# Kernel tuning notes

Hardware: AMD Instinct MI355X
Metric: run time of the kernel (lower is better)

Reference implementation:

```python
import jax, jax.numpy as jnp
import numpy as np

TOP_K = 2


def setup_inputs() -> dict:
    key = jax.random.key(0)
    kx, kw = jax.random.split(key)
    B, S, D, E = 4, 4096, 2048, 64
    x = jax.random.normal(kx, (B, S, D), dtype=jnp.float32)
    W = jax.random.normal(kw, (E, D), dtype=jnp.float32) * 0.02  # router weight [E, D]
    return {"x": x, "W": W}


def reference(x, W):
    B, S, D = x.shape
    E = W.shape[0]
    x_flat = x.reshape(-1, D)                      # [T, D], T = B*S
    router_logits = jnp.einsum('td,ed->te', x_flat, W)  # [T, E]
    router_probs = jax.nn.softmax(router_logits, axis=-1)
    expert_weights, expert_indices = jax.lax.top_k(router_probs, TOP_K)  # [T, K]
    expert_weights = expert_weights / jnp.sum(expert_weights, axis=-1, keepdims=True)
    expert_indices = expert_indices.reshape(B, S, TOP_K)
    expert_weights = expert_weights.reshape(B, S, TOP_K)
    # aux load-balance loss: sum((mean usage - 1/E)^2)
    expert_usage = jnp.mean(router_probs, axis=0)  # [E]
    aux_loss = jnp.sum((expert_usage - 1.0 / E) ** 2)
    return expert_indices, expert_weights, aux_loss
```

## Files before the change

### kernel.cpp

```cpp
#include <hip/hip_runtime.h>
#include <math.h>

#define T_TOK 16384
#define DDIM  2048
#define NE    64
#define NPLANE (NE * DDIM)
#define NBLK  512

typedef __attribute__((ext_vector_type(8))) short short8;
typedef __attribute__((ext_vector_type(4))) float floatx4;

union Frag8 { unsigned short u[8]; short8 v; };

__device__ __forceinline__ unsigned int bf16_rne_bits(float x) {
    unsigned int u = __builtin_bit_cast(unsigned int, x);
    return (u + 0x7fffu + ((u >> 16) & 1u)) & 0xffff0000u;
}

__device__ __forceinline__ void dma16(const float* g, float* lds) {
    __builtin_amdgcn_global_load_lds(
        (const __attribute__((address_space(1))) unsigned int*)g,
        (__attribute__((address_space(3))) unsigned int*)lds, 16, 0, 0);
}

__global__ void wsplit_kernel(const float* __restrict__ W,
                              unsigned short* __restrict__ wh,
                              unsigned short* __restrict__ wm,
                              unsigned short* __restrict__ wl) {
    int i = blockIdx.x * 256 + threadIdx.x;
    float w = W[i];
    unsigned int hb = bf16_rne_bits(w);
    float r  = w - __builtin_bit_cast(float, hb);
    unsigned int mb = bf16_rne_bits(r);
    float r2 = r - __builtin_bit_cast(float, mb);
    unsigned int lb = bf16_rne_bits(r2);
    wh[i] = (unsigned short)(hb >> 16);
    wm[i] = (unsigned short)(mb >> 16);
    wl[i] = (unsigned short)(lb >> 16);
}

__global__ __launch_bounds__(512, 4)
void router_main(const float* __restrict__ x,
                 const unsigned short* __restrict__ wh,
                 const unsigned short* __restrict__ wm,
                 const unsigned short* __restrict__ wl,
                 float* __restrict__ out, float* __restrict__ usage_part) {
    __shared__ float As[2 * 8192];
    __shared__ float ured[8][NE];
    float* lg = As;

    const int tid  = threadIdx.x;
    const int lane = tid & 63;
    const int wv   = __builtin_amdgcn_readfirstlane(tid >> 6);
    const int nh   = wv & 1;
    const int kq   = wv >> 1;
    const int cl   = lane & 15;
    const int q    = lane >> 4;
    const int t0   = blockIdx.x * 32;

    const float* xdma = x + (size_t)(t0 + (lane & 31)) * DDIM + kq * 512 + (lane >> 5) * 4;

    floatx4 acc[2][2];
#pragma unroll
    for (int mt = 0; mt < 2; ++mt)
#pragma unroll
        for (int nt = 0; nt < 2; ++nt)
            acc[mt][nt] = (floatx4){0.f, 0.f, 0.f, 0.f};

    const size_t bbase = (size_t)(nh * 32 + cl) * DDIM + kq * 512 + q * 8;

#pragma unroll
    for (int j = 0; j < 4; ++j) {
        const int k8 = nh * 4 + j;
        dma16(xdma + k8 * 8, As + kq * 2048 + k8 * 256);
    }

#pragma unroll 1
    for (int c = 0; c < 8; ++c) {
        __syncthreads();

        if (c + 1 < 8) {
            float* nb = As + ((c + 1) & 1) * 8192 + kq * 2048;
#pragma unroll
            for (int j = 0; j < 4; ++j) {
                const int k8 = nh * 4 + j;
                dma16(xdma + (c + 1) * 64 + k8 * 8, nb + k8 * 256);
            }
        }

        const float* buf = As + (c & 1) * 8192 + kq * 2048;

#pragma unroll
        for (int t = 0; t < 2; ++t) {
            const size_t bo = bbase + c * 64 + t * 32;
            uint4 cb[2][3];
#pragma unroll
            for (int nt = 0; nt < 2; ++nt) {
                const size_t o = bo + (size_t)nt * 16 * DDIM;
                cb[nt][0] = *(const uint4*)(wh + o);
                cb[nt][1] = *(const uint4*)(wm + o);
                cb[nt][2] = *(const uint4*)(wl + o);
            }
            short8 Ah[2], Am[2], Al[2];
#pragma unroll
            for (int mt = 0; mt < 2; ++mt) {
                const float* ap = buf + (t * 4 + q) * 256 + (mt * 16 + cl) * 4;
                float4 a0 = *(const float4*)(ap);
                float4 a1 = *(const float4*)(ap + 128);
                float f[8] = {a0.x, a0.y, a0.z, a0.w, a1.x, a1.y, a1.z, a1.w};
                Frag8 fh, fm, fl;
#pragma unroll
                for (int j = 0; j < 8; ++j) {
                    unsigned int ub = __builtin_bit_cast(unsigned int, f[j]);
                    unsigned int hb = ub & 0xffff0000u;
                    float r = f[j] - __builtin_bit_cast(float, hb);
                    unsigned int rb = __builtin_bit_cast(unsigned int, r);
                    unsigned int mb = rb & 0xffff0000u;
                    float r2 = r - __builtin_bit_cast(float, mb);
                    unsigned int lb = __builtin_bit_cast(unsigned int, r2);
                    fh.u[j] = (unsigned short)(hb >> 16);
                    fm.u[j] = (unsigned short)(mb >> 16);
                    fl.u[j] = (unsigned short)(lb >> 16);
                }
                Ah[mt] = fh.v; Am[mt] = fm.v; Al[mt] = fl.v;
            }

#pragma unroll
            for (int mt = 0; mt < 2; ++mt)
#pragma unroll
                for (int nt = 0; nt < 2; ++nt) {
                    short8 Bh = __builtin_bit_cast(short8, cb[nt][0]);
                    short8 Bm = __builtin_bit_cast(short8, cb[nt][1]);
                    short8 Bl = __builtin_bit_cast(short8, cb[nt][2]);
                    floatx4 a = acc[mt][nt];
                    a = __builtin_amdgcn_mfma_f32_16x16x32_bf16(Ah[mt], Bh, a, 0, 0, 0);
                    a = __builtin_amdgcn_mfma_f32_16x16x32_bf16(Ah[mt], Bm, a, 0, 0, 0);
                    a = __builtin_amdgcn_mfma_f32_16x16x32_bf16(Am[mt], Bh, a, 0, 0, 0);
                    a = __builtin_amdgcn_mfma_f32_16x16x32_bf16(Am[mt], Bm, a, 0, 0, 0);
                    a = __builtin_amdgcn_mfma_f32_16x16x32_bf16(Ah[mt], Bl, a, 0, 0, 0);
                    a = __builtin_amdgcn_mfma_f32_16x16x32_bf16(Al[mt], Bh, a, 0, 0, 0);
                    acc[mt][nt] = a;
                }
        }
    }

#pragma unroll
    for (int mt = 0; mt < 2; ++mt)
#pragma unroll
        for (int nt = 0; nt < 2; ++nt)
#pragma unroll
            for (int r = 0; r < 4; ++r)
                lg[kq * 2048 + (mt * 16 + q * 4 + r) * 64 + nh * 32 + nt * 16 + cl]
                    = acc[mt][nt][r];
    __syncthreads();

    float usage_acc = 0.f;
#pragma unroll 1
    for (int j = 0; j < 4; ++j) {
        const int tl = wv * 4 + j;
        const int t  = t0 + tl;
        float l = (lg[0 * 2048 + tl * 64 + lane] + lg[1 * 2048 + tl * 64 + lane]) +
                  (lg[2 * 2048 + tl * 64 + lane] + lg[3 * 2048 + tl * 64 + lane]);

        float v1 = l; int i1 = lane;
#pragma unroll
        for (int off = 32; off >= 1; off >>= 1) {
            float ov = __shfl_xor(v1, off, 64);
            int   oi = __shfl_xor(i1, off, 64);
            if (ov > v1 || (ov == v1 && oi < i1)) { v1 = ov; i1 = oi; }
        }
        float lm = (lane == i1) ? -INFINITY : l;
        float v2 = lm; int i2 = lane;
#pragma unroll
        for (int off = 32; off >= 1; off >>= 1) {
            float ov = __shfl_xor(v2, off, 64);
            int   oi = __shfl_xor(i2, off, 64);
            if (ov > v2 || (ov == v2 && oi < i2)) { v2 = ov; i2 = oi; }
        }

        float p = expf(l - v1);
        float s = p;
#pragma unroll
        for (int off = 32; off >= 1; off >>= 1) s += __shfl_xor(s, off, 64);

        float e2  = expf(v2 - v1);
        float rcp = 1.0f / (1.0f + e2);
        usage_acc += p / s;

        if (lane == 0) {
            out[(size_t)t * 2 + 0]         = (float)i1;
            out[(size_t)t * 2 + 1]         = (float)i2;
            out[32768 + (size_t)t * 2 + 0] = rcp;
            out[32768 + (size_t)t * 2 + 1] = e2 * rcp;
        }
    }

    ured[wv][lane] = usage_acc;
    __syncthreads();
    if (wv == 0) {
        float s = ((ured[0][lane] + ured[1][lane]) + (ured[2][lane] + ured[3][lane])) +
                  ((ured[4][lane] + ured[5][lane]) + (ured[6][lane] + ured[7][lane]));
        usage_part[(size_t)blockIdx.x * 64 + lane] = s;
    }
}

__global__ __launch_bounds__(1024)
void router_aux(const float* __restrict__ usage_part, float* __restrict__ out) {
    __shared__ float red[16][NE];
    const int tid = threadIdx.x;
    const int e   = tid & 63;
    const int g   = tid >> 6;
    float s = 0.f;
#pragma unroll
    for (int i = 0; i < NBLK / 16; ++i)
        s += usage_part[(size_t)(g * (NBLK / 16) + i) * 64 + e];
    red[g][e] = s;
    __syncthreads();
    if (g == 0) {
        float tot = 0.f;
#pragma unroll
        for (int i = 0; i < 16; ++i) tot += red[i][e];
        float u = tot * (1.0f / 16384.0f) - (1.0f / 64.0f);
        float sq = u * u;
#pragma unroll
        for (int off = 32; off >= 1; off >>= 1) sq += __shfl_xor(sq, off, 64);
        if (e == 0) out[65536] = sq;
    }
}

extern "C" void kernel_launch(void* const* d_in, const int* in_sizes, int n_in,
                              void* d_out, int out_size, void* d_ws, size_t ws_size,
                              hipStream_t stream) {
    const float* x = (const float*)d_in[0];
    const float* W = (const float*)d_in[1];
    float* out     = (float*)d_out;

    unsigned short* ws_h = (unsigned short*)d_ws;
    unsigned short* ws_m = ws_h + NPLANE;
    unsigned short* ws_l = ws_m + NPLANE;
    float* upart         = (float*)(ws_l + NPLANE);

    wsplit_kernel<<<dim3(NPLANE / 256), dim3(256), 0, stream>>>(W, ws_h, ws_m, ws_l);
    router_main<<<dim3(NBLK), dim3(512), 0, stream>>>(x, ws_h, ws_m, ws_l, out, upart);
    router_aux<<<dim3(1), dim3(1024), 0, stream>>>(upart, out);
}
```

Baseline: 234.8 us.

## Load x directly from global into registers with 8-way K split per wave

Removes the LDS double-buffered global_load_lds staging of x and the per-chunk block barriers. Each of the 8 waves now owns a 256-wide K slice, reads its A fragments straight from global memory, and covers all 64 experts with a 2x4 accumulator tile. The 8 per-wave partial logits are then summed through LDS. This trades barrier and LDS traffic for uncoalesced 32-byte-per-lane global reads of x with no software prefetch, more accumulator registers, and a fully unrolled loop.

Result: slower. 243.8 us (+3.8%).

```diff
diff --git a/kernel.cpp b/kernel.cpp
--- a/kernel.cpp
+++ b/kernel.cpp
@@ -15,12 +15,6 @@
 __device__ __forceinline__ unsigned int bf16_rne_bits(float x) {
     unsigned int u = __builtin_bit_cast(unsigned int, x);
     return (u + 0x7fffu + ((u >> 16) & 1u)) & 0xffff0000u;
-}
-
-__device__ __forceinline__ void dma16(const float* g, float* lds) {
-    __builtin_amdgcn_global_load_lds(
-        (const __attribute__((address_space(1))) unsigned int*)g,
-        (__attribute__((address_space(3))) unsigned int*)lds, 16, 0, 0);
 }
 
 __global__ void wsplit_kernel(const float* __restrict__ W,
@@ -45,112 +39,88 @@
                  const unsigned short* __restrict__ wm,
                  const unsigned short* __restrict__ wl,
                  float* __restrict__ out, float* __restrict__ usage_part) {
-    __shared__ float As[2 * 8192];
+    __shared__ float lg[8 * 2048];
     __shared__ float ured[8][NE];
-    float* lg = As;
 
     const int tid  = threadIdx.x;
     const int lane = tid & 63;
     const int wv   = __builtin_amdgcn_readfirstlane(tid >> 6);
-    const int nh   = wv & 1;
-    const int kq   = wv >> 1;
     const int cl   = lane & 15;
     const int q    = lane >> 4;
     const int t0   = blockIdx.x * 32;
 
-    const float* xdma = x + (size_t)(t0 + (lane & 31)) * DDIM + kq * 512 + (lane >> 5) * 4;
-
-    floatx4 acc[2][2];
+    const float* xa = x + (size_t)(t0 + cl) * DDIM + wv * 256 + q * 8;
+    const size_t bb = (size_t)cl * DDIM + wv * 256 + q * 8;
+
+    floatx4 acc[2][4];
 #pragma unroll
     for (int mt = 0; mt < 2; ++mt)
 #pragma unroll
-        for (int nt = 0; nt < 2; ++nt)
+        for (int nt = 0; nt < 4; ++nt)
             acc[mt][nt] = (floatx4){0.f, 0.f, 0.f, 0.f};
 
-    const size_t bbase = (size_t)(nh * 32 + cl) * DDIM + kq * 512 + q * 8;
-
-#pragma unroll
-    for (int j = 0; j < 4; ++j) {
-        const int k8 = nh * 4 + j;
-        dma16(xdma + k8 * 8, As + kq * 2048 + k8 * 256);
-    }
-
-#pragma unroll 1
+#pragma unroll
     for (int c = 0; c < 8; ++c) {
-        __syncthreads();
-
-        if (c + 1 < 8) {
-            float* nb = As + ((c + 1) & 1) * 8192 + kq * 2048;
-#pragma unroll
-            for (int j = 0; j < 4; ++j) {
-                const int k8 = nh * 4 + j;
-                dma16(xdma + (c + 1) * 64 + k8 * 8, nb + k8 * 256);
+        const int ko = c * 32;
+
+        uint4 cb[4][3];
+#pragma unroll
+        for (int nt = 0; nt < 4; ++nt) {
+            const size_t o = bb + (size_t)nt * 16 * DDIM + ko;
+            cb[nt][0] = *(const uint4*)(wh + o);
+            cb[nt][1] = *(const uint4*)(wm + o);
+            cb[nt][2] = *(const uint4*)(wl + o);
+        }
+
+        short8 Ah[2], Am[2], Al[2];
+#pragma unroll
+        for (int mt = 0; mt < 2; ++mt) {
+            const float* ap = xa + (size_t)mt * 16 * DDIM + ko;
+            float4 a0 = *(const float4*)(ap);
+            float4 a1 = *(const float4*)(ap + 4);
+            float f[8] = {a0.x, a0.y, a0.z, a0.w, a1.x, a1.y, a1.z, a1.w};
+            Frag8 fh, fm, fl;
+#pragma unroll
+            for (int j = 0; j < 8; ++j) {
+                unsigned int ub = __builtin_bit_cast(unsigned int, f[j]);
+                unsigned int hb = ub & 0xffff0000u;
+                float r = f[j] - __builtin_bit_cast(float, hb);
+                unsigned int rb = __builtin_bit_cast(unsigned int, r);
+                unsigned int mb = rb & 0xffff0000u;
+                float r2 = r - __builtin_bit_cast(float, mb);
+                unsigned int lb = __builtin_bit_cast(unsigned int, r2);
+                fh.u[j] = (unsigned short)(hb >> 16);
+                fm.u[j] = (unsigned short)(mb >> 16);
+                fl.u[j] = (unsigned short)(lb >> 16);
             }
-        }
-
-        const float* buf = As + (c & 1) * 8192 + kq * 2048;
-
-#pragma unroll
-        for (int t = 0; t < 2; ++t) {
-            const size_t bo = bbase + c * 64 + t * 32;
-            uint4 cb[2][3];
-#pragma unroll
-            for (int nt = 0; nt < 2; ++nt) {
-                const size_t o = bo + (size_t)nt * 16 * DDIM;
-                cb[nt][0] = *(const uint4*)(wh + o);
-                cb[nt][1] = *(const uint4*)(wm + o);
-                cb[nt][2] = *(const uint4*)(wl + o);
+            Ah[mt] = fh.v; Am[mt] = fm.v; Al[mt] = fl.v;
+        }
+
+#pragma unroll
+        for (int mt = 0; mt < 2; ++mt)
+#pragma unroll
+            for (int nt = 0; nt < 4; ++nt) {
+                short8 Bh = __builtin_bit_cast(short8, cb[nt][0]);
+                short8 Bm = __builtin_bit_cast(short8, cb[nt][1]);
+                short8 Bl = __builtin_bit_cast(short8, cb[nt][2]);
+                floatx4 a = acc[mt][nt];
+                a = __builtin_amdgcn_mfma_f32_16x16x32_bf16(Ah[mt], Bh, a, 0, 0, 0);
+                a = __builtin_amdgcn_mfma_f32_16x16x32_bf16(Ah[mt], Bm, a, 0, 0, 0);
+                a = __builtin_amdgcn_mfma_f32_16x16x32_bf16(Am[mt], Bh, a, 0, 0, 0);
+                a = __builtin_amdgcn_mfma_f32_16x16x32_bf16(Am[mt], Bm, a, 0, 0, 0);
+                a = __builtin_amdgcn_mfma_f32_16x16x32_bf16(Ah[mt], Bl, a, 0, 0, 0);
+                a = __builtin_amdgcn_mfma_f32_16x16x32_bf16(Al[mt], Bh, a, 0, 0, 0);
+                acc[mt][nt] = a;
             }
-            short8 Ah[2], Am[2], Al[2];
-#pragma unroll
-            for (int mt = 0; mt < 2; ++mt) {
-                const float* ap = buf + (t * 4 + q) * 256 + (mt * 16 + cl) * 4;
-                float4 a0 = *(const float4*)(ap);
-                float4 a1 = *(const float4*)(ap + 128);
-                float f[8] = {a0.x, a0.y, a0.z, a0.w, a1.x, a1.y, a1.z, a1.w};
-                Frag8 fh, fm, fl;
-#pragma unroll
-                for (int j = 0; j < 8; ++j) {
-                    unsigned int ub = __builtin_bit_cast(unsigned int, f[j]);
-                    unsigned int hb = ub & 0xffff0000u;
-                    float r = f[j] - __builtin_bit_cast(float, hb);
-                    unsigned int rb = __builtin_bit_cast(unsigned int, r);
-                    unsigned int mb = rb & 0xffff0000u;
-                    float r2 = r - __builtin_bit_cast(float, mb);
-                    unsigned int lb = __builtin_bit_cast(unsigned int, r2);
-                    fh.u[j] = (unsigned short)(hb >> 16);
-                    fm.u[j] = (unsigned short)(mb >> 16);
-                    fl.u[j] = (unsigned short)(lb >> 16);
-                }
-                Ah[mt] = fh.v; Am[mt] = fm.v; Al[mt] = fl.v;
-            }
-
-#pragma unroll
-            for (int mt = 0; mt < 2; ++mt)
-#pragma unroll
-                for (int nt = 0; nt < 2; ++nt) {
-                    short8 Bh = __builtin_bit_cast(short8, cb[nt][0]);
-                    short8 Bm = __builtin_bit_cast(short8, cb[nt][1]);
-                    short8 Bl = __builtin_bit_cast(short8, cb[nt][2]);
-                    floatx4 a = acc[mt][nt];
-                    a = __builtin_amdgcn_mfma_f32_16x16x32_bf16(Ah[mt], Bh, a, 0, 0, 0);
-                    a = __builtin_amdgcn_mfma_f32_16x16x32_bf16(Ah[mt], Bm, a, 0, 0, 0);
-                    a = __builtin_amdgcn_mfma_f32_16x16x32_bf16(Am[mt], Bh, a, 0, 0, 0);
-                    a = __builtin_amdgcn_mfma_f32_16x16x32_bf16(Am[mt], Bm, a, 0, 0, 0);
-                    a = __builtin_amdgcn_mfma_f32_16x16x32_bf16(Ah[mt], Bl, a, 0, 0, 0);
-                    a = __builtin_amdgcn_mfma_f32_16x16x32_bf16(Al[mt], Bh, a, 0, 0, 0);
-                    acc[mt][nt] = a;
-                }
-        }
     }
 
 #pragma unroll
     for (int mt = 0; mt < 2; ++mt)
 #pragma unroll
-        for (int nt = 0; nt < 2; ++nt)
+        for (int nt = 0; nt < 4; ++nt)
 #pragma unroll
             for (int r = 0; r < 4; ++r)
-                lg[kq * 2048 + (mt * 16 + q * 4 + r) * 64 + nh * 32 + nt * 16 + cl]
+                lg[wv * 2048 + (mt * 16 + q * 4 + r) * 64 + nt * 16 + cl]
                     = acc[mt][nt][r];
     __syncthreads();
 
@@ -159,8 +129,10 @@
     for (int j = 0; j < 4; ++j) {
         const int tl = wv * 4 + j;
         const int t  = t0 + tl;
-        float l = (lg[0 * 2048 + tl * 64 + lane] + lg[1 * 2048 + tl * 64 + lane]) +
-                  (lg[2 * 2048 + tl * 64 + lane] + lg[3 * 2048 + tl * 64 + lane]);
+        float l = (((lg[0 * 2048 + tl * 64 + lane] + lg[1 * 2048 + tl * 64 + lane]) +
+                    (lg[2 * 2048 + tl * 64 + lane] + lg[3 * 2048 + tl * 64 + lane])) +
+                   ((lg[4 * 2048 + tl * 64 + lane] + lg[5 * 2048 + tl * 64 + lane]) +
+                    (lg[6 * 2048 + tl * 64 + lane] + lg[7 * 2048 + tl * 64 + lane])));
 
         float v1 = l; int i1 = lane;
 #pragma unroll
```

## Split K across sixteen waves per block with 1024-thread router blocks

Applied to the files above, without the earlier changes.

Doubles the router block to 1024 threads, splitting the 2048-wide reduction into eight K slices of 256 instead of four slices of 512. Each wave now issues half as many MFMA steps and DMA loads per chunk, which raises the number of waves in flight per CU to hide latency. The logits epilogue sums eight partial slices, each wave handles two tokens, and a barrier is added before reusing the staging buffer. The costs are a larger cross-wave LDS reduction and tighter register limits from the new launch bounds, which may cause spilling.

Measured after the change: 240.2 us. 2.3% more time.

```diff
diff --git a/kernel.cpp b/kernel.cpp
--- a/kernel.cpp
+++ b/kernel.cpp
@@ -39,14 +39,14 @@
     wl[i] = (unsigned short)(lb >> 16);
 }
 
-__global__ __launch_bounds__(512, 4)
+__global__ __launch_bounds__(1024, 8)
 void router_main(const float* __restrict__ x,
                  const unsigned short* __restrict__ wh,
                  const unsigned short* __restrict__ wm,
                  const unsigned short* __restrict__ wl,
                  float* __restrict__ out, float* __restrict__ usage_part) {
     __shared__ float As[2 * 8192];
-    __shared__ float ured[8][NE];
+    __shared__ float ured[16][NE];
     float* lg = As;
 
     const int tid  = threadIdx.x;
@@ -58,7 +58,7 @@
     const int q    = lane >> 4;
     const int t0   = blockIdx.x * 32;
 
-    const float* xdma = x + (size_t)(t0 + (lane & 31)) * DDIM + kq * 512 + (lane >> 5) * 4;
+    const float* xdma = x + (size_t)(t0 + (lane & 31)) * DDIM + kq * 256 + (lane >> 5) * 4;
 
     floatx4 acc[2][2];
 #pragma unroll
@@ -67,12 +67,12 @@
         for (int nt = 0; nt < 2; ++nt)
             acc[mt][nt] = (floatx4){0.f, 0.f, 0.f, 0.f};
 
-    const size_t bbase = (size_t)(nh * 32 + cl) * DDIM + kq * 512 + q * 8;
-
-#pragma unroll
-    for (int j = 0; j < 4; ++j) {
-        const int k8 = nh * 4 + j;
-        dma16(xdma + k8 * 8, As + kq * 2048 + k8 * 256);
+    const size_t bbase = (size_t)(nh * 32 + cl) * DDIM + kq * 256 + q * 8;
+
+#pragma unroll
+    for (int g2 = 0; g2 < 2; ++g2) {
+        const int g = nh * 2 + g2;
+        dma16(xdma + g * 8, As + kq * 1024 + g * 256);
     }
 
 #pragma unroll 1
@@ -80,69 +80,68 @@
         __syncthreads();
 
         if (c + 1 < 8) {
-            float* nb = As + ((c + 1) & 1) * 8192 + kq * 2048;
-#pragma unroll
-            for (int j = 0; j < 4; ++j) {
-                const int k8 = nh * 4 + j;
-                dma16(xdma + (c + 1) * 64 + k8 * 8, nb + k8 * 256);
+            float* nb = As + ((c + 1) & 1) * 8192 + kq * 1024;
+#pragma unroll
+            for (int g2 = 0; g2 < 2; ++g2) {
+                const int g = nh * 2 + g2;
+                dma16(xdma + (c + 1) * 32 + g * 8, nb + g * 256);
             }
         }
 
-        const float* buf = As + (c & 1) * 8192 + kq * 2048;
-
-#pragma unroll
-        for (int t = 0; t < 2; ++t) {
-            const size_t bo = bbase + c * 64 + t * 32;
-            uint4 cb[2][3];
+        const float* buf = As + (c & 1) * 8192 + kq * 1024;
+
+        const size_t bo = bbase + c * 32;
+        uint4 cb[2][3];
+#pragma unroll
+        for (int nt = 0; nt < 2; ++nt) {
+            const size_t o = bo + (size_t)nt * 16 * DDIM;
+            cb[nt][0] = *(const uint4*)(wh + o);
+            cb[nt][1] = *(const uint4*)(wm + o);
+            cb[nt][2] = *(const uint4*)(wl + o);
+        }
+        short8 Ah[2], Am[2], Al[2];
+#pragma unroll
+        for (int mt = 0; mt < 2; ++mt) {
+            const float* ap = buf + q * 256 + (mt * 16 + cl) * 4;
+            float4 a0 = *(const float4*)(ap);
+            float4 a1 = *(const float4*)(ap + 128);
+            float f[8] = {a0.x, a0.y, a0.z, a0.w, a1.x, a1.y, a1.z, a1.w};
+            Frag8 fh, fm, fl;
+#pragma unroll
+            for (int j = 0; j < 8; ++j) {
+                unsigned int ub = __builtin_bit_cast(unsigned int, f[j]);
+                unsigned int hb = ub & 0xffff0000u;
+                float r = f[j] - __builtin_bit_cast(float, hb);
+                unsigned int rb = __builtin_bit_cast(unsigned int, r);
+                unsigned int mb = rb & 0xffff0000u;
+                float r2 = r - __builtin_bit_cast(float, mb);
+                unsigned int lb = __builtin_bit_cast(unsigned int, r2);
+                fh.u[j] = (unsigned short)(hb >> 16);
+                fm.u[j] = (unsigned short)(mb >> 16);
+                fl.u[j] = (unsigned short)(lb >> 16);
+            }
+            Ah[mt] = fh.v; Am[mt] = fm.v; Al[mt] = fl.v;
+        }
+
+#pragma unroll
+        for (int mt = 0; mt < 2; ++mt)
 #pragma unroll
             for (int nt = 0; nt < 2; ++nt) {
-                const size_t o = bo + (size_t)nt * 16 * DDIM;
-                cb[nt][0] = *(const uint4*)(wh + o);
-                cb[nt][1] = *(const uint4*)(wm + o);
-                cb[nt][2] = *(const uint4*)(wl + o);
+                short8 Bh = __builtin_bit_cast(short8, cb[nt][0]);
+                short8 Bm = __builtin_bit_cast(short8, cb[nt][1]);
+                short8 Bl = __builtin_bit_cast(short8, cb[nt][2]);
+                floatx4 a = acc[mt][nt];
+                a = __builtin_amdgcn_mfma_f32_16x16x32_bf16(Ah[mt], Bh, a, 0, 0, 0);
+                a = __builtin_amdgcn_mfma_f32_16x16x32_bf16(Ah[mt], Bm, a, 0, 0, 0);
+                a = __builtin_amdgcn_mfma_f32_16x16x32_bf16(Am[mt], Bh, a, 0, 0, 0);
+                a = __builtin_amdgcn_mfma_f32_16x16x32_bf16(Am[mt], Bm, a, 0, 0, 0);
+                a = __builtin_amdgcn_mfma_f32_16x16x32_bf16(Ah[mt], Bl, a, 0, 0, 0);
+                a = __builtin_amdgcn_mfma_f32_16x16x32_bf16(Al[mt], Bh, a, 0, 0, 0);
+                acc[mt][nt] = a;
             }
-            short8 Ah[2], Am[2], Al[2];
-#pragma unroll
-            for (int mt = 0; mt < 2; ++mt) {
-                const float* ap = buf + (t * 4 + q) * 256 + (mt * 16 + cl) * 4;
-                float4 a0 = *(const float4*)(ap);
-                float4 a1 = *(const float4*)(ap + 128);
-                float f[8] = {a0.x, a0.y, a0.z, a0.w, a1.x, a1.y, a1.z, a1.w};
-                Frag8 fh, fm, fl;
-#pragma unroll
-                for (int j = 0; j < 8; ++j) {
-                    unsigned int ub = __builtin_bit_cast(unsigned int, f[j]);
-                    unsigned int hb = ub & 0xffff0000u;
-                    float r = f[j] - __builtin_bit_cast(float, hb);
-                    unsigned int rb = __builtin_bit_cast(unsigned int, r);
-                    unsigned int mb = rb & 0xffff0000u;
-                    float r2 = r - __builtin_bit_cast(float, mb);
-                    unsigned int lb = __builtin_bit_cast(unsigned int, r2);
-                    fh.u[j] = (unsigned short)(hb >> 16);
-                    fm.u[j] = (unsigned short)(mb >> 16);
-                    fl.u[j] = (unsigned short)(lb >> 16);
-                }
-                Ah[mt] = fh.v; Am[mt] = fm.v; Al[mt] = fl.v;
-            }
-
-#pragma unroll
-            for (int mt = 0; mt < 2; ++mt)
-#pragma unroll
-                for (int nt = 0; nt < 2; ++nt) {
-                    short8 Bh = __builtin_bit_cast(short8, cb[nt][0]);
-                    short8 Bm = __builtin_bit_cast(short8, cb[nt][1]);
-                    short8 Bl = __builtin_bit_cast(short8, cb[nt][2]);
-                    floatx4 a = acc[mt][nt];
-                    a = __builtin_amdgcn_mfma_f32_16x16x32_bf16(Ah[mt], Bh, a, 0, 0, 0);
-                    a = __builtin_amdgcn_mfma_f32_16x16x32_bf16(Ah[mt], Bm, a, 0, 0, 0);
-                    a = __builtin_amdgcn_mfma_f32_16x16x32_bf16(Am[mt], Bh, a, 0, 0, 0);
-                    a = __builtin_amdgcn_mfma_f32_16x16x32_bf16(Am[mt], Bm, a, 0, 0, 0);
-                    a = __builtin_amdgcn_mfma_f32_16x16x32_bf16(Ah[mt], Bl, a, 0, 0, 0);
-                    a = __builtin_amdgcn_mfma_f32_16x16x32_bf16(Al[mt], Bh, a, 0, 0, 0);
-                    acc[mt][nt] = a;
-                }
-        }
-    }
+    }
+
+    __syncthreads();
 
 #pragma unroll
     for (int mt = 0; mt < 2; ++mt)
@@ -156,11 +155,13 @@
 
     float usage_acc = 0.f;
 #pragma unroll 1
-    for (int j = 0; j < 4; ++j) {
-        const int tl = wv * 4 + j;
+    for (int j = 0; j < 2; ++j) {
+        const int tl = wv * 2 + j;
         const int t  = t0 + tl;
-        float l = (lg[0 * 2048 + tl * 64 + lane] + lg[1 * 2048 + tl * 64 + lane]) +
-                  (lg[2 * 2048 + tl * 64 + lane] + lg[3 * 2048 + tl * 64 + lane]);
+        float l = (((lg[0 * 2048 + tl * 64 + lane] + lg[1 * 2048 + tl * 64 + lane]) +
+                    (lg[2 * 2048 + tl * 64 + lane] + lg[3 * 2048 + tl * 64 + lane])) +
+                   ((lg[4 * 2048 + tl * 64 + lane] + lg[5 * 2048 + tl * 64 + lane]) +
+                    (lg[6 * 2048 + tl * 64 + lane] + lg[7 * 2048 + tl * 64 + lane])));
 
         float v1 = l; int i1 = lane;
 #pragma unroll
@@ -198,8 +199,10 @@
     ured[wv][lane] = usage_acc;
     __syncthreads();
     if (wv == 0) {
-        float s = ((ured[0][lane] + ured[1][lane]) + (ured[2][lane] + ured[3][lane])) +
-                  ((ured[4][lane] + ured[5][lane]) + (ured[6][lane] + ured[7][lane]));
+        float s = (((ured[0][lane] + ured[1][lane]) + (ured[2][lane] + ured[3][lane])) +
+                   ((ured[4][lane] + ured[5][lane]) + (ured[6][lane] + ured[7][lane]))) +
+                  (((ured[8][lane] + ured[9][lane]) + (ured[10][lane] + ured[11][lane])) +
+                   ((ured[12][lane] + ured[13][lane]) + (ured[14][lane] + ured[15][lane])));
         usage_part[(size_t)blockIdx.x * 64 + lane] = s;
     }
 }
@@ -241,6 +244,6 @@
     float* upart         = (float*)(ws_l + NPLANE);
 
     wsplit_kernel<<<dim3(NPLANE / 256), dim3(256), 0, stream>>>(W, ws_h, ws_m, ws_l);
-    router_main<<<dim3(NBLK), dim3(512), 0, stream>>>(x, ws_h, ws_m, ws_l, out, upart);
+    router_main<<<dim3(NBLK), dim3(1024), 0, stream>>>(x, ws_h, ws_m, ws_l, out, upart);
     router_aux<<<dim3(1), dim3(1024), 0, stream>>>(upart, out);
 }
```
